# Optimization experiments

Hardware: AMD Instinct MI355X
Metric: run time of the kernel (lower is better)

## Reference

```python
import jax, jax.numpy as jnp
import numpy as np

NUM_GRAPHS = 1024

def setup_inputs() -> dict:
    key = jax.random.key(0)
    ks = jax.random.split(key, 6)
    N, E = 500000, 16000000
    x = jax.random.normal(ks[0], (N, 4), dtype=jnp.float32)
    edge_index = jax.random.randint(ks[1], (2, E), 0, N, dtype=jnp.int32)
    batch = jnp.sort(jax.random.randint(ks[2], (N,), 0, NUM_GRAPHS, dtype=jnp.int32))
    eps = jnp.zeros((), dtype=jnp.float32)
    W1 = jax.random.normal(ks[3], (4, 16), dtype=jnp.float32) * 0.5
    b1 = jnp.zeros((16,), dtype=jnp.float32)
    W2 = jax.random.normal(ks[4], (16, 4), dtype=jnp.float32) * 0.25
    b2 = jnp.zeros((4,), dtype=jnp.float32)
    return {"x": x, "edge_index": edge_index, "batch": batch,
            "eps": eps, "W1": W1, "b1": b1, "W2": W2, "b2": b2}

def reference(x, edge_index, batch, eps, W1, b1, W2, b2):
    N = x.shape[0]
    src, dst = edge_index[0], edge_index[1]
    # GINConv aggregation: sum of neighbor (source) features at each target node
    agg = jax.ops.segment_sum(x[src], dst, num_segments=N)  # [N, 4]
    h = (1.0 + eps) * x + agg
    # 2-layer MLP: Lin(4,16) -> ReLU -> Lin(16,4)
    h = jax.nn.relu(h @ W1 + b1) @ W2 + b2
    h = jax.nn.relu(h)
    # global_mean_pool over batch segment ids
    sums = jax.ops.segment_sum(h, batch, num_segments=NUM_GRAPHS)      # [G, 4]
    cnts = jax.ops.segment_sum(jnp.ones((N,), h.dtype), batch, num_segments=NUM_GRAPHS)
    pooled = sums / jnp.maximum(cnts, 1.0)[:, None]
    return jax.nn.log_softmax(pooled, axis=1)
```

## Files before the change

kernel.cpp:

```cpp
#include <hip/hip_runtime.h>

#define NUM_GRAPHS 1024
#define BIN_BITS 10
#define BIN_SIZE (1 << BIN_BITS)
#define EB 4096
#define STH 512
#define EPT 8
#define SWAVES 8
#define CURS 16
#define ACCTH 256
#define ACCW 4

typedef int v4i __attribute__((ext_vector_type(4)));

__device__ inline unsigned bf16_rn(float f) {
    unsigned u = __float_as_uint(f);
    return (u + 0x7FFFu + ((u >> 16) & 1u)) >> 16;
}
__global__ void prep_kernel(const float4* __restrict__ x, uint2* __restrict__ x16,
                            int N) {
    int i = blockIdx.x * blockDim.x + threadIdx.x;
    if (i < N) {
        float4 v = x[i];
        uint2 r;
        r.x = bf16_rn(v.x) | (bf16_rn(v.y) << 16);
        r.y = bf16_rn(v.z) | (bf16_rn(v.w) << 16);
        x16[i] = r;
    }
}

__global__ void __launch_bounds__(STH, 6) bin_scatter(const int* __restrict__ src,
                                                      const int* __restrict__ dst,
                                                      int* __restrict__ packed,
                                                      int* __restrict__ cursor,
                                                      int E, int cap, int nb) {
    __shared__ int hist[SWAVES][512];
    __shared__ int wbase[SWAVES][512];

    const int t = threadIdx.x;
    const int lane = t & 63;
    const int wave = t >> 6;
    const int b0 = blockIdx.x * EB;
    const int myBase = b0 + t * EPT;

    for (int j = t; j < SWAVES * 512; j += STH) (&hist[0][0])[j] = 0;
    __syncthreads();

    int dbuf[EPT], sbuf[EPT];
    const bool full = (myBase + EPT <= E);
    if (full) {
        *(int4*)(dbuf)     = *(const int4*)(dst + myBase);
        *(int4*)(dbuf + 4) = *(const int4*)(dst + myBase + 4);
        *(int4*)(sbuf)     = *(const int4*)(src + myBase);
        *(int4*)(sbuf + 4) = *(const int4*)(src + myBase + 4);
    } else {
#pragma unroll
        for (int i = 0; i < EPT; ++i) {
            int e = myBase + i;
            bool ok = e < E;
            dbuf[i] = ok ? dst[e] : 0;
            sbuf[i] = ok ? src[e] : 0;
        }
    }

    int pv[EPT];
    int bnlp[EPT];
#pragma unroll
    for (int k = 0; k < EPT; ++k) {
        int e = myBase + k;
        bool ok = full || (e < E);
        int d = dbuf[k];
        int bn = ((unsigned)d) >> BIN_BITS;
        pv[k] = ((d & (BIN_SIZE - 1)) << 19) | sbuf[k];
        unsigned long long m = __ballot(ok);
#pragma unroll
        for (int bb = 0; bb < 9; ++bb) {
            unsigned long long bm = __ballot((bn >> bb) & 1);
            m &= ((bn >> bb) & 1) ? bm : ~bm;
        }
        int rank = (int)__popcll(m & ((1ull << lane) - 1ull));
        int cnt  = (int)__popcll(m);
        int leader = __ffsll((unsigned long long)m) - 1;
        int old = hist[wave][bn];
        if (ok && lane == leader) hist[wave][bn] = old + cnt;
        bnlp[k] = ok ? ((bn << 16) | (old + rank)) : -1;
    }
    __syncthreads();

    {
        int c[SWAVES];
        int total = 0;
#pragma unroll
        for (int w = 0; w < SWAVES; ++w) { c[w] = hist[w][t]; total += c[w]; }
        int base = t * cap;
        if (t < nb && total > 0) base += atomicAdd(&cursor[t * CURS], total);
        int acc = base;
#pragma unroll
        for (int w = 0; w < SWAVES; ++w) { wbase[w][t] = acc; acc += c[w]; }
    }
    __syncthreads();

    if (full) {
#pragma unroll
        for (int k = 0; k < EPT; ++k) {
            int bn = ((unsigned)bnlp[k]) >> 16;
            int lp = bnlp[k] & 0xFFFF;
            int pos = wbase[wave][bn] + lp;
            if (pos < (bn + 1) * cap)
                packed[pos] = pv[k];
        }
    } else {
#pragma unroll
        for (int k = 0; k < EPT; ++k) {
            if (bnlp[k] >= 0) {
                int bn = ((unsigned)bnlp[k]) >> 16;
                int lp = bnlp[k] & 0xFFFF;
                int pos = wbase[wave][bn] + lp;
                if (pos < (bn + 1) * cap)
                    packed[pos] = pv[k];
            }
        }
    }
}

#define LOADR(B, PE, VM) do {                                              \
    int _i = (B) + lane * 4;                                               \
    if (_i + 3 < s1) {                                                     \
        v4i _p4 = __builtin_nontemporal_load((const v4i*)(packed + _i));   \
        PE[0] = _p4.x; PE[1] = _p4.y; PE[2] = _p4.z; PE[3] = _p4.w;        \
        VM = 0xF;                                                          \
    } else {                                                               \
        VM = 0;                                                            \
        PE[0] = (_i + 0 < s1) ? (VM |= 1, packed[_i + 0]) : 0;             \
        PE[1] = (_i + 1 < s1) ? (VM |= 2, packed[_i + 1]) : 0;             \
        PE[2] = (_i + 2 < s1) ? (VM |= 4, packed[_i + 2]) : 0;             \
        PE[3] = (_i + 3 < s1) ? (VM |= 8, packed[_i + 3]) : 0;             \
    }                                                                      \
} while (0)

#define GATHR(PE, G) do {                                                  \
    G[0] = x16[PE[0] & 0x7FFFF];                                           \
    G[1] = x16[PE[1] & 0x7FFFF];                                           \
    G[2] = x16[PE[2] & 0x7FFFF];                                           \
    G[3] = x16[PE[3] & 0x7FFFF];                                           \
} while (0)

#define PROCR(PE, G, VM) do {                                              \
    _Pragma("unroll")                                                      \
    for (int k = 0; k < 4; ++k) {                                          \
        int p = PE[k];                                                     \
        int dl = (((unsigned)p) >> 19) & (BIN_SIZE - 1);                   \
        unsigned long long m = ~0ull;                                      \
        _Pragma("unroll")                                                  \
        for (int bb = 0; bb < BIN_BITS; ++bb) {                            \
            unsigned long long bm = __ballot((dl >> bb) & 1);              \
            m &= ((dl >> bb) & 1) ? bm : ~bm;                              \
        }                                                                  \
        int rank = (int)__popcll(m & ((1ull << lane) - 1ull));             \
        float sc = ((VM >> k) & 1) ? 1.0f : 0.0f;                          \
        float v0 = __uint_as_float(G[k].x << 16) * sc;                     \
        float v1 = __uint_as_float(G[k].x & 0xFFFF0000u) * sc;             \
        float v2 = __uint_as_float(G[k].y << 16) * sc;                     \
        float v3 = __uint_as_float(G[k].y & 0xFFFF0000u) * sc;             \
        float4* pp = (float4*)&planes[wave][dl][0];                        \
        for (int pass = 0; __any(rank >= pass); ++pass) {                  \
            if (rank == pass) {                                            \
                float4 a = *pp;                                            \
                a.x += v0; a.y += v1; a.z += v2; a.w += v3;                \
                *pp = a;                                                   \
            }                                                              \
        }                                                                  \
    }                                                                      \
} while (0)

__global__ void __launch_bounds__(ACCTH) bin_accum_mlp_pool(
        const float4* __restrict__ x,
        const uint2* __restrict__ x16,
        const int* __restrict__ packed,
        const int* __restrict__ cursor,
        const int* __restrict__ batch,
        const float* __restrict__ eps_p,
        const float* __restrict__ W1, const float* __restrict__ b1,
        const float* __restrict__ W2, const float* __restrict__ b2,
        float* __restrict__ gsum, float* __restrict__ gcnt,
        int N, int cap) {
    __shared__ float planes[ACCW][BIN_SIZE][4];

    const int bin = blockIdx.x;
    const int t = threadIdx.x;
    const int lane = t & 63;
    const int wave = t >> 6;

    {
        float4* pz = (float4*)&planes[0][0][0];
        float4 z; z.x = 0.f; z.y = 0.f; z.z = 0.f; z.w = 0.f;
#pragma unroll
        for (int i = 0; i < 16; ++i) pz[t + i * ACCTH] = z;
    }
    __syncthreads();

    const int start = bin * cap;
    int cnt = cursor[bin * CURS];
    if (cnt > cap) cnt = cap;
    if (cnt < 0) cnt = 0;
    const int end = start + cnt;

    int seg = ((cnt + ACCW - 1) / ACCW + 3) & ~3;
    int s0 = start + wave * seg;
    int s1 = s0 + seg; if (s1 > end) s1 = end;

    if (s0 < s1) {
        int peA[4], peB[4], vmA, vmB;
        uint2 gA[4], gB[4];
        int b = s0;
        LOADR(b, peA, vmA);
        GATHR(peA, gA);
        for (;;) {
            int b1n = b + 256;
            if (b1n < s1) { LOADR(b1n, peB, vmB); GATHR(peB, gB); }
            PROCR(peA, gA, vmA);
            if (b1n >= s1) break;
            int b2n = b1n + 256;
            if (b2n < s1) { LOADR(b2n, peA, vmA); GATHR(peA, gA); }
            PROCR(peB, gB, vmB);
            if (b2n >= s1) break;
            b = b2n;
        }
    }
    __syncthreads();

    const float eps = eps_p[0];
    for (int half = 0; half < 4; ++half) {
        int node = t + half * ACCTH;
        float4 a = *(const float4*)&planes[0][node][0];
#pragma unroll
        for (int w = 1; w < ACCW; ++w) {
            float4 bq = *(const float4*)&planes[w][node][0];
            a.x += bq.x; a.y += bq.y; a.z += bq.z; a.w += bq.w;
        }

        int n = bin * BIN_SIZE + node;
        bool valid = n < N;
        float o0 = 0.f, o1 = 0.f, o2 = 0.f, o3 = 0.f;
        int g = -1;
        if (valid) {
            float4 xv = x[n];
            float h0 = (1.0f + eps) * xv.x + a.x;
            float h1 = (1.0f + eps) * xv.y + a.y;
            float h2 = (1.0f + eps) * xv.z + a.z;
            float h3 = (1.0f + eps) * xv.w + a.w;

            float tmp[16];
#pragma unroll
            for (int j = 0; j < 16; ++j) {
                float v = b1[j] + h0 * W1[j] + h1 * W1[16 + j] + h2 * W1[32 + j] + h3 * W1[48 + j];
                tmp[j] = v > 0.0f ? v : 0.0f;
            }
            float o[4];
#pragma unroll
            for (int j = 0; j < 4; ++j) {
                float v = b2[j];
#pragma unroll
                for (int k = 0; k < 16; ++k) v += tmp[k] * W2[k * 4 + j];
                o[j] = v > 0.0f ? v : 0.0f;
            }
            o0 = o[0]; o1 = o[1]; o2 = o[2]; o3 = o[3];
            g = batch[n];
        }

        int g0 = __shfl(g, 0);
        bool uni = __all(g == g0);
        if (uni && g0 >= 0) {
#pragma unroll
            for (int off = 32; off > 0; off >>= 1) {
                o0 += __shfl_down(o0, off);
                o1 += __shfl_down(o1, off);
                o2 += __shfl_down(o2, off);
                o3 += __shfl_down(o3, off);
            }
            if (lane == 0) {
                unsafeAtomicAdd(&gsum[(size_t)g0 * 4 + 0], o0);
                unsafeAtomicAdd(&gsum[(size_t)g0 * 4 + 1], o1);
                unsafeAtomicAdd(&gsum[(size_t)g0 * 4 + 2], o2);
                unsafeAtomicAdd(&gsum[(size_t)g0 * 4 + 3], o3);
                unsafeAtomicAdd(&gcnt[g0], 64.0f);
            }
        } else if (valid) {
            unsafeAtomicAdd(&gsum[(size_t)g * 4 + 0], o0);
            unsafeAtomicAdd(&gsum[(size_t)g * 4 + 1], o1);
            unsafeAtomicAdd(&gsum[(size_t)g * 4 + 2], o2);
            unsafeAtomicAdd(&gsum[(size_t)g * 4 + 3], o3);
            unsafeAtomicAdd(&gcnt[g], 1.0f);
        }
    }
}

__global__ void pool_softmax_kernel(const float* __restrict__ gsum,
                                    const float* __restrict__ gcnt,
                                    float* __restrict__ out) {
    int g = blockIdx.x * blockDim.x + threadIdx.x;
    if (g >= NUM_GRAPHS) return;
    float c = fmaxf(gcnt[g], 1.0f);
    float p0 = gsum[g * 4 + 0] / c;
    float p1 = gsum[g * 4 + 1] / c;
    float p2 = gsum[g * 4 + 2] / c;
    float p3 = gsum[g * 4 + 3] / c;
    float m = fmaxf(fmaxf(p0, p1), fmaxf(p2, p3));
    float s = expf(p0 - m) + expf(p1 - m) + expf(p2 - m) + expf(p3 - m);
    float lse = m + logf(s);
    out[g * 4 + 0] = p0 - lse;
    out[g * 4 + 1] = p1 - lse;
    out[g * 4 + 2] = p2 - lse;
    out[g * 4 + 3] = p3 - lse;
}

__global__ void edge_scatter_kernel(const float4* __restrict__ x,
                                    const int* __restrict__ src,
                                    const int* __restrict__ dst,
                                    float* __restrict__ agg,
                                    int E) {
    int t = blockIdx.x * blockDim.x + threadIdx.x;
    int e = t * 4;
    if (e + 3 < E) {
        int4 s = *(const int4*)(src + e);
        int4 d = *(const int4*)(dst + e);
        float4 xv;
        xv = x[s.x];
        unsafeAtomicAdd(&agg[(size_t)d.x * 4 + 0], xv.x);
        unsafeAtomicAdd(&agg[(size_t)d.x * 4 + 1], xv.y);
        unsafeAtomicAdd(&agg[(size_t)d.x * 4 + 2], xv.z);
        unsafeAtomicAdd(&agg[(size_t)d.x * 4 + 3], xv.w);
        xv = x[s.y];
        unsafeAtomicAdd(&agg[(size_t)d.y * 4 + 0], xv.x);
        unsafeAtomicAdd(&agg[(size_t)d.y * 4 + 1], xv.y);
        unsafeAtomicAdd(&agg[(size_t)d.y * 4 + 2], xv.z);
        unsafeAtomicAdd(&agg[(size_t)d.y * 4 + 3], xv.w);
        xv = x[s.z];
        unsafeAtomicAdd(&agg[(size_t)d.z * 4 + 0], xv.x);
        unsafeAtomicAdd(&agg[(size_t)d.z * 4 + 1], xv.y);
        unsafeAtomicAdd(&agg[(size_t)d.z * 4 + 2], xv.z);
        unsafeAtomicAdd(&agg[(size_t)d.z * 4 + 3], xv.w);
        xv = x[s.w];
        unsafeAtomicAdd(&agg[(size_t)d.w * 4 + 0], xv.x);
        unsafeAtomicAdd(&agg[(size_t)d.w * 4 + 1], xv.y);
        unsafeAtomicAdd(&agg[(size_t)d.w * 4 + 2], xv.z);
        unsafeAtomicAdd(&agg[(size_t)d.w * 4 + 3], xv.w);
    } else {
        for (int i = e; i < E; ++i) {
            int sv = src[i], dv = dst[i];
            float4 xv = x[sv];
            unsafeAtomicAdd(&agg[(size_t)dv * 4 + 0], xv.x);
            unsafeAtomicAdd(&agg[(size_t)dv * 4 + 1], xv.y);
            unsafeAtomicAdd(&agg[(size_t)dv * 4 + 2], xv.z);
            unsafeAtomicAdd(&agg[(size_t)dv * 4 + 3], xv.w);
        }
    }
}

__global__ void node_mlp_pool_kernel(const float4* __restrict__ x,
                                     const float4* __restrict__ agg,
                                     const int* __restrict__ batch,
                                     const float* __restrict__ eps_p,
                                     const float* __restrict__ W1,
                                     const float* __restrict__ b1,
                                     const float* __restrict__ W2,
                                     const float* __restrict__ b2,
                                     float* __restrict__ gsum,
                                     float* __restrict__ gcnt,
                                     int N) {
    int i = blockIdx.x * blockDim.x + threadIdx.x;
    bool valid = i < N;
    float o0 = 0.f, o1 = 0.f, o2 = 0.f, o3 = 0.f;
    int g = -1;
    if (valid) {
        float eps = eps_p[0];
        float4 xv = x[i];
        float4 av = agg[i];
        float h0 = (1.0f + eps) * xv.x + av.x;
        float h1 = (1.0f + eps) * xv.y + av.y;
        float h2 = (1.0f + eps) * xv.z + av.z;
        float h3 = (1.0f + eps) * xv.w + av.w;
        float tmp[16];
#pragma unroll
        for (int j = 0; j < 16; ++j) {
            float v = b1[j] + h0 * W1[j] + h1 * W1[16 + j] + h2 * W1[32 + j] + h3 * W1[48 + j];
            tmp[j] = v > 0.0f ? v : 0.0f;
        }
        float o[4];
#pragma unroll
        for (int j = 0; j < 4; ++j) {
            float v = b2[j];
#pragma unroll
            for (int k = 0; k < 16; ++k) v += tmp[k] * W2[k * 4 + j];
            o[j] = v > 0.0f ? v : 0.0f;
        }
        o0 = o[0]; o1 = o[1]; o2 = o[2]; o3 = o[3];
        g = batch[i];
    }
    int g0 = __shfl(g, 0);
    bool uni = __all(g == g0);
    if (uni && g0 >= 0) {
#pragma unroll
        for (int off = 32; off > 0; off >>= 1) {
            o0 += __shfl_down(o0, off);
            o1 += __shfl_down(o1, off);
            o2 += __shfl_down(o2, off);
            o3 += __shfl_down(o3, off);
        }
        if ((threadIdx.x & 63) == 0) {
            unsafeAtomicAdd(&gsum[(size_t)g0 * 4 + 0], o0);
            unsafeAtomicAdd(&gsum[(size_t)g0 * 4 + 1], o1);
            unsafeAtomicAdd(&gsum[(size_t)g0 * 4 + 2], o2);
            unsafeAtomicAdd(&gsum[(size_t)g0 * 4 + 3], o3);
            unsafeAtomicAdd(&gcnt[g0], 64.0f);
        }
    } else if (valid) {
        unsafeAtomicAdd(&gsum[(size_t)g * 4 + 0], o0);
        unsafeAtomicAdd(&gsum[(size_t)g * 4 + 1], o1);
        unsafeAtomicAdd(&gsum[(size_t)g * 4 + 2], o2);
        unsafeAtomicAdd(&gsum[(size_t)g * 4 + 3], o3);
        unsafeAtomicAdd(&gcnt[g], 1.0f);
    }
}

extern "C" void kernel_launch(void* const* d_in, const int* in_sizes, int n_in,
                              void* d_out, int out_size, void* d_ws, size_t ws_size,
                              hipStream_t stream) {
    const float* x     = (const float*)d_in[0];
    const int*   ei    = (const int*)d_in[1];
    const int*   batch = (const int*)d_in[2];
    const float* eps   = (const float*)d_in[3];
    const float* W1    = (const float*)d_in[4];
    const float* b1    = (const float*)d_in[5];
    const float* W2    = (const float*)d_in[6];
    const float* b2    = (const float*)d_in[7];

    const int N = in_sizes[0] / 4;
    const int E = in_sizes[1] / 2;
    const int* src = ei;
    const int* dst = ei + (size_t)E;

    const int nb = (N + BIN_SIZE - 1) >> BIN_BITS;
    const int epb = (E + nb - 1) / nb;
    int cap = epb + epb / 8 + 1024;
    cap = (cap + 3) & ~3;

    size_t x16_elems = ((size_t)2 * N + 3) & ~(size_t)3;
    size_t packed_elems = ((size_t)nb * cap + 3) & ~(size_t)3;
    size_t need = (x16_elems + packed_elems + 512 * CURS + NUM_GRAPHS * 5) * sizeof(float);

    if (nb <= 512 && N < (1 << 19) && need <= ws_size) {
        uint2* x16    = (uint2*)d_ws;
        int*   packed = (int*)d_ws + x16_elems;
        int*   cursor = packed + packed_elems;
        float* gsum   = (float*)(cursor + 512 * CURS);
        float* gcnt   = gsum + (size_t)NUM_GRAPHS * 4;

        (void)hipMemsetAsync(cursor, 0,
                             (512 * CURS + NUM_GRAPHS * 5) * sizeof(int), stream);

        prep_kernel<<<(N + 511) / 512, 512, 0, stream>>>((const float4*)x, x16, N);

        int nblocks_e = (E + EB - 1) / EB;
        bin_scatter<<<nblocks_e, STH, 0, stream>>>(src, dst, packed, cursor, E, cap, nb);

        bin_accum_mlp_pool<<<nb, ACCTH, 0, stream>>>(
            (const float4*)x, (const uint2*)x16, packed, cursor, batch, eps,
            W1, b1, W2, b2, gsum, gcnt, N, cap);

        pool_softmax_kernel<<<(NUM_GRAPHS + 255) / 256, 256, 0, stream>>>(
            gsum, gcnt, (float*)d_out);
    } else {
        float* agg  = (float*)d_ws;
        float* gsum = agg + (size_t)N * 4;
        float* gcnt = gsum + (size_t)NUM_GRAPHS * 4;
        size_t zero_bytes = ((size_t)N * 4 + NUM_GRAPHS * 5) * sizeof(float);
        (void)hipMemsetAsync(d_ws, 0, zero_bytes, stream);

        int e4 = (E + 3) / 4;
        edge_scatter_kernel<<<(e4 + 255) / 256, 256, 0, stream>>>(
            (const float4*)x, src, dst, agg, E);

        node_mlp_pool_kernel<<<(N + 255) / 256, 256, 0, stream>>>(
            (const float4*)x, (const float4*)agg, batch, eps, W1, b1, W2, b2,
            gsum, gcnt, N);

        pool_softmax_kernel<<<(NUM_GRAPHS + 255) / 256, 256, 0, stream>>>(
            gsum, gcnt, (float*)d_out);
    }
}
```

Baseline: 432.8 us.

## Fuse bf16 prep into bin_scatter and pre-reduce same-bin adds via shuffles

The separate prep kernel that converts x to packed bf16 is folded into the first threads of bin_scatter, removing one kernel launch. In the accumulation macro, lanes that share a destination row now combine their values with wave shuffles, so only the leader lane writes to shared memory. This replaces the previous serialized rank-by-rank LDS update loop. It adds shuffle-loop iterations proportional to the conflict count and a guard requiring enough scatter blocks to cover N.

```diff
diff --git a/kernel.cpp b/kernel.cpp
--- a/kernel.cpp
+++ b/kernel.cpp
@@ -17,23 +17,14 @@
     unsigned u = __float_as_uint(f);
     return (u + 0x7FFFu + ((u >> 16) & 1u)) >> 16;
 }
-__global__ void prep_kernel(const float4* __restrict__ x, uint2* __restrict__ x16,
-                            int N) {
-    int i = blockIdx.x * blockDim.x + threadIdx.x;
-    if (i < N) {
-        float4 v = x[i];
-        uint2 r;
-        r.x = bf16_rn(v.x) | (bf16_rn(v.y) << 16);
-        r.y = bf16_rn(v.z) | (bf16_rn(v.w) << 16);
-        x16[i] = r;
-    }
-}
-
-__global__ void __launch_bounds__(STH, 6) bin_scatter(const int* __restrict__ src,
+
+__global__ void __launch_bounds__(STH, 6) bin_scatter(const float4* __restrict__ x,
+                                                      uint2* __restrict__ x16,
+                                                      const int* __restrict__ src,
                                                       const int* __restrict__ dst,
                                                       int* __restrict__ packed,
                                                       int* __restrict__ cursor,
-                                                      int E, int cap, int nb) {
+                                                      int N, int E, int cap, int nb) {
     __shared__ int hist[SWAVES][512];
     __shared__ int wbase[SWAVES][512];
 
@@ -42,6 +33,17 @@
     const int wave = t >> 6;
     const int b0 = blockIdx.x * EB;
     const int myBase = b0 + t * EPT;
+
+    {
+        int nd = blockIdx.x * STH + t;
+        if (nd < N) {
+            float4 v = x[nd];
+            uint2 r;
+            r.x = bf16_rn(v.x) | (bf16_rn(v.y) << 16);
+            r.y = bf16_rn(v.z) | (bf16_rn(v.w) << 16);
+            x16[nd] = r;
+        }
+    }
 
     for (int j = t; j < SWAVES * 512; j += STH) (&hist[0][0])[j] = 0;
     __syncthreads();
@@ -162,13 +164,23 @@
         float v1 = __uint_as_float(G[k].x & 0xFFFF0000u) * sc;             \
         float v2 = __uint_as_float(G[k].y << 16) * sc;                     \
         float v3 = __uint_as_float(G[k].y & 0xFFFF0000u) * sc;             \
-        float4* pp = (float4*)&planes[wave][dl][0];                        \
-        for (int pass = 0; __any(rank >= pass); ++pass) {                  \
-            if (rank == pass) {                                            \
-                float4 a = *pp;                                            \
-                a.x += v0; a.y += v1; a.z += v2; a.w += v3;                \
-                *pp = a;                                                   \
-            }                                                              \
+                      \
+        unsigned long long rem =                                           \
+            (rank == 0) ? (m & ~(1ull << lane)) : 0ull;                    \
+        while (__any(rem != 0)) {                                          \
+            int srcl = rem ? (__ffsll((unsigned long long)rem) - 1) : 0;   \
+            float t0 = __shfl(v0, srcl);                                   \
+            float t1 = __shfl(v1, srcl);                                   \
+            float t2 = __shfl(v2, srcl);                                   \
+            float t3 = __shfl(v3, srcl);                                   \
+            if (rem) { v0 += t0; v1 += t1; v2 += t2; v3 += t3;             \
+                       rem &= rem - 1; }                                   \
+        }                                                                  \
+        if (rank == 0) {                                                   \
+            float4* pp = (float4*)&planes[wave][dl][0];                    \
+            float4 a = *pp;                                                \
+            a.x += v0; a.y += v1; a.z += v2; a.w += v3;                    \
+            *pp = a;                                                       \
         }                                                                  \
     }                                                                      \
 } while (0)
@@ -449,7 +461,10 @@
     size_t packed_elems = ((size_t)nb * cap + 3) & ~(size_t)3;
     size_t need = (x16_elems + packed_elems + 512 * CURS + NUM_GRAPHS * 5) * sizeof(float);
 
-    if (nb <= 512 && N < (1 << 19) && need <= ws_size) {
+    int nblocks_e = (E + EB - 1) / EB;
+    bool prep_ok = (size_t)nblocks_e * STH >= (size_t)N;
+
+    if (nb <= 512 && N < (1 << 19) && need <= ws_size && prep_ok) {
         uint2* x16    = (uint2*)d_ws;
         int*   packed = (int*)d_ws + x16_elems;
         int*   cursor = packed + packed_elems;
@@ -459,10 +474,8 @@
         (void)hipMemsetAsync(cursor, 0,
                              (512 * CURS + NUM_GRAPHS * 5) * sizeof(int), stream);
 
-        prep_kernel<<<(N + 511) / 512, 512, 0, stream>>>((const float4*)x, x16, N);
-
-        int nblocks_e = (E + EB - 1) / EB;
-        bin_scatter<<<nblocks_e, STH, 0, stream>>>(src, dst, packed, cursor, E, cap, nb);
+        bin_scatter<<<nblocks_e, STH, 0, stream>>>(
+            (const float4*)x, x16, src, dst, packed, cursor, N, E, cap, nb);
 
         bin_accum_mlp_pool<<<nb, ACCTH, 0, stream>>>(
             (const float4*)x, (const uint2*)x16, packed, cursor, batch, eps,
```

Result: no change. 429.6 us (-0.7%).

## Fuse GIN pipeline into one cooperative persistent kernel with grid syncs

Applied to the files above, without the earlier changes.

Replaces the memset, prep, binning scatter, accumulation and softmax launches with a single cooperative kernel. It uses grid-wide syncs between the phases and loops over chunks and bins persistently. This removes launch and memset overhead and inter-kernel gaps. In exchange, the persistent grid is capped at occupancy (at most 512 blocks), scatter runs with 4 waves per chunk instead of 8, and the double-buffered gather prefetch in accumulation is dropped. The non-cooperative fallback also folds the bf16 prep into bin_scatter.

```diff
diff --git a/kernel.cpp b/kernel.cpp
--- a/kernel.cpp
+++ b/kernel.cpp
@@ -1,126 +1,25 @@
 #include <hip/hip_runtime.h>
+#include <hip/hip_cooperative_groups.h>
+namespace cg = cooperative_groups;
 
 #define NUM_GRAPHS 1024
 #define BIN_BITS 10
 #define BIN_SIZE (1 << BIN_BITS)
+#define CURS 16
 #define EB 4096
 #define STH 512
 #define EPT 8
 #define SWAVES 8
-#define CURS 16
 #define ACCTH 256
 #define ACCW 4
+#define FEPT 8
+#define FCHK (ACCTH * FEPT)
 
 typedef int v4i __attribute__((ext_vector_type(4)));
 
 __device__ inline unsigned bf16_rn(float f) {
     unsigned u = __float_as_uint(f);
     return (u + 0x7FFFu + ((u >> 16) & 1u)) >> 16;
-}
-__global__ void prep_kernel(const float4* __restrict__ x, uint2* __restrict__ x16,
-                            int N) {
-    int i = blockIdx.x * blockDim.x + threadIdx.x;
-    if (i < N) {
-        float4 v = x[i];
-        uint2 r;
-        r.x = bf16_rn(v.x) | (bf16_rn(v.y) << 16);
-        r.y = bf16_rn(v.z) | (bf16_rn(v.w) << 16);
-        x16[i] = r;
-    }
-}
-
-__global__ void __launch_bounds__(STH, 6) bin_scatter(const int* __restrict__ src,
-                                                      const int* __restrict__ dst,
-                                                      int* __restrict__ packed,
-                                                      int* __restrict__ cursor,
-                                                      int E, int cap, int nb) {
-    __shared__ int hist[SWAVES][512];
-    __shared__ int wbase[SWAVES][512];
-
-    const int t = threadIdx.x;
-    const int lane = t & 63;
-    const int wave = t >> 6;
-    const int b0 = blockIdx.x * EB;
-    const int myBase = b0 + t * EPT;
-
-    for (int j = t; j < SWAVES * 512; j += STH) (&hist[0][0])[j] = 0;
-    __syncthreads();
-
-    int dbuf[EPT], sbuf[EPT];
-    const bool full = (myBase + EPT <= E);
-    if (full) {
-        *(int4*)(dbuf)     = *(const int4*)(dst + myBase);
-        *(int4*)(dbuf + 4) = *(const int4*)(dst + myBase + 4);
-        *(int4*)(sbuf)     = *(const int4*)(src + myBase);
-        *(int4*)(sbuf + 4) = *(const int4*)(src + myBase + 4);
-    } else {
-#pragma unroll
-        for (int i = 0; i < EPT; ++i) {
-            int e = myBase + i;
-            bool ok = e < E;
-            dbuf[i] = ok ? dst[e] : 0;
-            sbuf[i] = ok ? src[e] : 0;
-        }
-    }
-
-    int pv[EPT];
-    int bnlp[EPT];
-#pragma unroll
-    for (int k = 0; k < EPT; ++k) {
-        int e = myBase + k;
-        bool ok = full || (e < E);
-        int d = dbuf[k];
-        int bn = ((unsigned)d) >> BIN_BITS;
-        pv[k] = ((d & (BIN_SIZE - 1)) << 19) | sbuf[k];
-        unsigned long long m = __ballot(ok);
-#pragma unroll
-        for (int bb = 0; bb < 9; ++bb) {
-            unsigned long long bm = __ballot((bn >> bb) & 1);
-            m &= ((bn >> bb) & 1) ? bm : ~bm;
-        }
-        int rank = (int)__popcll(m & ((1ull << lane) - 1ull));
-        int cnt  = (int)__popcll(m);
-        int leader = __ffsll((unsigned long long)m) - 1;
-        int old = hist[wave][bn];
-        if (ok && lane == leader) hist[wave][bn] = old + cnt;
-        bnlp[k] = ok ? ((bn << 16) | (old + rank)) : -1;
-    }
-    __syncthreads();
-
-    {
-        int c[SWAVES];
-        int total = 0;
-#pragma unroll
-        for (int w = 0; w < SWAVES; ++w) { c[w] = hist[w][t]; total += c[w]; }
-        int base = t * cap;
-        if (t < nb && total > 0) base += atomicAdd(&cursor[t * CURS], total);
-        int acc = base;
-#pragma unroll
-        for (int w = 0; w < SWAVES; ++w) { wbase[w][t] = acc; acc += c[w]; }
-    }
-    __syncthreads();
-
-    if (full) {
-#pragma unroll
-        for (int k = 0; k < EPT; ++k) {
-            int bn = ((unsigned)bnlp[k]) >> 16;
-            int lp = bnlp[k] & 0xFFFF;
-            int pos = wbase[wave][bn] + lp;
-            if (pos < (bn + 1) * cap)
-                packed[pos] = pv[k];
-        }
-    } else {
-#pragma unroll
-        for (int k = 0; k < EPT; ++k) {
-            if (bnlp[k] >= 0) {
-                int bn = ((unsigned)bnlp[k]) >> 16;
-                int lp = bnlp[k] & 0xFFFF;
-                int pos = wbase[wave][bn] + lp;
-                if (pos < (bn + 1) * cap)
-                    packed[pos] = pv[k];
-            }
-        }
-    }
 }
 
 #define LOADR(B, PE, VM) do {                                              \
@@ -173,6 +72,345 @@
     }                                                                      \
 } while (0)
 
+__global__ void __launch_bounds__(ACCTH) fused_gin(
+        const float4* __restrict__ x, uint2* __restrict__ x16,
+        const int* __restrict__ src, const int* __restrict__ dst,
+        int* __restrict__ packed, int* __restrict__ cursor,
+        const int* __restrict__ batch, const float* __restrict__ eps_p,
+        const float* __restrict__ W1, const float* __restrict__ b1,
+        const float* __restrict__ W2, const float* __restrict__ b2,
+        float* __restrict__ gsum, float* __restrict__ gcnt,
+        float* __restrict__ out,
+        int N, int E, int cap, int nb) {
+    cg::grid_group grid = cg::this_grid();
+    __shared__ float planes[ACCW][BIN_SIZE][4];
+    int* hist  = (int*)&planes[0][0][0];
+    int* wbase = hist + ACCW * 512;
+
+    const int t = threadIdx.x;
+    const int lane = t & 63;
+    const int wave = t >> 6;
+    const int nblk = gridDim.x;
+    const int gid0 = blockIdx.x * ACCTH + t;
+    const int gstr = nblk * ACCTH;
+
+    for (int i = gid0; i < 512; i += gstr) cursor[i * CURS] = 0;
+    for (int i = gid0; i < NUM_GRAPHS * 4; i += gstr) gsum[i] = 0.0f;
+    for (int i = gid0; i < NUM_GRAPHS; i += gstr) gcnt[i] = 0.0f;
+    for (int i = gid0; i < N; i += gstr) {
+        float4 v = x[i];
+        uint2 r;
+        r.x = bf16_rn(v.x) | (bf16_rn(v.y) << 16);
+        r.y = bf16_rn(v.z) | (bf16_rn(v.w) << 16);
+        x16[i] = r;
+    }
+    grid.sync();
+
+    const int nchunks = (E + FCHK - 1) / FCHK;
+    for (int ch = blockIdx.x; ch < nchunks; ch += nblk) {
+        const int b0 = ch * FCHK;
+        const int myBase = b0 + t * FEPT;
+
+        for (int j = t; j < ACCW * 512; j += ACCTH) hist[j] = 0;
+        __syncthreads();
+
+        int dbuf[FEPT], sbuf[FEPT];
+        const bool full = (myBase + FEPT <= E);
+        if (full) {
+            *(int4*)(dbuf)     = *(const int4*)(dst + myBase);
+            *(int4*)(dbuf + 4) = *(const int4*)(dst + myBase + 4);
+            *(int4*)(sbuf)     = *(const int4*)(src + myBase);
+            *(int4*)(sbuf + 4) = *(const int4*)(src + myBase + 4);
+        } else {
+#pragma unroll
+            for (int i = 0; i < FEPT; ++i) {
+                int e = myBase + i;
+                bool ok = e < E;
+                dbuf[i] = ok ? dst[e] : 0;
+                sbuf[i] = ok ? src[e] : 0;
+            }
+        }
+
+        int pv[FEPT], bnlp[FEPT];
+#pragma unroll
+        for (int k = 0; k < FEPT; ++k) {
+            int e = myBase + k;
+            bool ok = full || (e < E);
+            int d = dbuf[k];
+            int bn = ((unsigned)d) >> BIN_BITS;
+            pv[k] = ((d & (BIN_SIZE - 1)) << 19) | sbuf[k];
+            unsigned long long m = __ballot(ok);
+#pragma unroll
+            for (int bb = 0; bb < 9; ++bb) {
+                unsigned long long bm = __ballot((bn >> bb) & 1);
+                m &= ((bn >> bb) & 1) ? bm : ~bm;
+            }
+            int rank = (int)__popcll(m & ((1ull << lane) - 1ull));
+            int cnt  = (int)__popcll(m);
+            int leader = __ffsll((unsigned long long)m) - 1;
+            int old = hist[wave * 512 + bn];
+            if (ok && lane == leader) hist[wave * 512 + bn] = old + cnt;
+            bnlp[k] = ok ? ((bn << 16) | (old + rank)) : -1;
+        }
+        __syncthreads();
+
+        for (int j = t; j < 512; j += ACCTH) {
+            int c0 = hist[0 * 512 + j], c1 = hist[1 * 512 + j];
+            int c2 = hist[2 * 512 + j], c3 = hist[3 * 512 + j];
+            int total = c0 + c1 + c2 + c3;
+            int base = j * cap;
+            if (j < nb && total > 0) base += atomicAdd(&cursor[j * CURS], total);
+            wbase[0 * 512 + j] = base;
+            wbase[1 * 512 + j] = base + c0;
+            wbase[2 * 512 + j] = base + c0 + c1;
+            wbase[3 * 512 + j] = base + c0 + c1 + c2;
+        }
+        __syncthreads();
+
+        if (full) {
+#pragma unroll
+            for (int k = 0; k < FEPT; ++k) {
+                int bn = ((unsigned)bnlp[k]) >> 16;
+                int lp = bnlp[k] & 0xFFFF;
+                int pos = wbase[wave * 512 + bn] + lp;
+                if (pos < (bn + 1) * cap)
+                    packed[pos] = pv[k];
+            }
+        } else {
+#pragma unroll
+            for (int k = 0; k < FEPT; ++k) {
+                if (bnlp[k] >= 0) {
+                    int bn = ((unsigned)bnlp[k]) >> 16;
+                    int lp = bnlp[k] & 0xFFFF;
+                    int pos = wbase[wave * 512 + bn] + lp;
+                    if (pos < (bn + 1) * cap)
+                        packed[pos] = pv[k];
+                }
+            }
+        }
+        __syncthreads();
+    }
+    __threadfence();
+    grid.sync();
+
+    for (int bin = blockIdx.x; bin < nb; bin += nblk) {
+        {
+            float4 z; z.x = 0.f; z.y = 0.f; z.z = 0.f; z.w = 0.f;
+            float4* pz = (float4*)&planes[0][0][0];
+#pragma unroll
+            for (int i = 0; i < 16; ++i) pz[t + i * ACCTH] = z;
+        }
+        __syncthreads();
+
+        const int startb = bin * cap;
+        int cnt = cursor[bin * CURS];
+        if (cnt > cap) cnt = cap;
+        if (cnt < 0) cnt = 0;
+        const int endb = startb + cnt;
+        int seg = ((cnt + ACCW - 1) / ACCW + 3) & ~3;
+        int s0 = startb + wave * seg;
+        int s1 = s0 + seg; if (s1 > endb) s1 = endb;
+
+        for (int b = s0; b < s1; b += 256) {
+            int pe[4]; int vm; uint2 g[4];
+            LOADR(b, pe, vm);
+            GATHR(pe, g);
+            PROCR(pe, g, vm);
+        }
+        __syncthreads();
+
+        const float eps = eps_p[0];
+        for (int hb = 0; hb < 4; ++hb) {
+            int node = t + hb * ACCTH;
+            float4 a = *(const float4*)&planes[0][node][0];
+#pragma unroll
+            for (int w = 1; w < ACCW; ++w) {
+                float4 bq = *(const float4*)&planes[w][node][0];
+                a.x += bq.x; a.y += bq.y; a.z += bq.z; a.w += bq.w;
+            }
+
+            int n = bin * BIN_SIZE + node;
+            bool valid = n < N;
+            float o0 = 0.f, o1 = 0.f, o2 = 0.f, o3 = 0.f;
+            int g = -1;
+            if (valid) {
+                float4 xv = x[n];
+                float h0 = (1.0f + eps) * xv.x + a.x;
+                float h1 = (1.0f + eps) * xv.y + a.y;
+                float h2 = (1.0f + eps) * xv.z + a.z;
+                float h3 = (1.0f + eps) * xv.w + a.w;
+
+                float tmp[16];
+#pragma unroll
+                for (int j = 0; j < 16; ++j) {
+                    float v = b1[j] + h0 * W1[j] + h1 * W1[16 + j] + h2 * W1[32 + j] + h3 * W1[48 + j];
+                    tmp[j] = v > 0.0f ? v : 0.0f;
+                }
+                float o[4];
+#pragma unroll
+                for (int j = 0; j < 4; ++j) {
+                    float v = b2[j];
+#pragma unroll
+                    for (int k = 0; k < 16; ++k) v += tmp[k] * W2[k * 4 + j];
+                    o[j] = v > 0.0f ? v : 0.0f;
+                }
+                o0 = o[0]; o1 = o[1]; o2 = o[2]; o3 = o[3];
+                g = batch[n];
+            }
+
+            int g0 = __shfl(g, 0);
+            bool uni = __all(g == g0);
+            if (uni && g0 >= 0) {
+#pragma unroll
+                for (int off = 32; off > 0; off >>= 1) {
+                    o0 += __shfl_down(o0, off);
+                    o1 += __shfl_down(o1, off);
+                    o2 += __shfl_down(o2, off);
+                    o3 += __shfl_down(o3, off);
+                }
+                if (lane == 0) {
+                    unsafeAtomicAdd(&gsum[(size_t)g0 * 4 + 0], o0);
+                    unsafeAtomicAdd(&gsum[(size_t)g0 * 4 + 1], o1);
+                    unsafeAtomicAdd(&gsum[(size_t)g0 * 4 + 2], o2);
+                    unsafeAtomicAdd(&gsum[(size_t)g0 * 4 + 3], o3);
+                    unsafeAtomicAdd(&gcnt[g0], 64.0f);
+                }
+            } else if (valid) {
+                unsafeAtomicAdd(&gsum[(size_t)g * 4 + 0], o0);
+                unsafeAtomicAdd(&gsum[(size_t)g * 4 + 1], o1);
+                unsafeAtomicAdd(&gsum[(size_t)g * 4 + 2], o2);
+                unsafeAtomicAdd(&gsum[(size_t)g * 4 + 3], o3);
+                unsafeAtomicAdd(&gcnt[g], 1.0f);
+            }
+        }
+        __syncthreads();
+    }
+    __threadfence();
+    grid.sync();
+
+    for (int g = gid0; g < NUM_GRAPHS; g += gstr) {
+        float c = fmaxf(unsafeAtomicAdd(&gcnt[g], 0.0f), 1.0f);
+        float p0 = unsafeAtomicAdd(&gsum[g * 4 + 0], 0.0f) / c;
+        float p1 = unsafeAtomicAdd(&gsum[g * 4 + 1], 0.0f) / c;
+        float p2 = unsafeAtomicAdd(&gsum[g * 4 + 2], 0.0f) / c;
+        float p3 = unsafeAtomicAdd(&gsum[g * 4 + 3], 0.0f) / c;
+        float m = fmaxf(fmaxf(p0, p1), fmaxf(p2, p3));
+        float s = expf(p0 - m) + expf(p1 - m) + expf(p2 - m) + expf(p3 - m);
+        float lse = m + logf(s);
+        out[g * 4 + 0] = p0 - lse;
+        out[g * 4 + 1] = p1 - lse;
+        out[g * 4 + 2] = p2 - lse;
+        out[g * 4 + 3] = p3 - lse;
+    }
+}
+
+__global__ void __launch_bounds__(STH, 6) bin_scatter(const float4* __restrict__ x,
+                                                      uint2* __restrict__ x16,
+                                                      const int* __restrict__ src,
+                                                      const int* __restrict__ dst,
+                                                      int* __restrict__ packed,
+                                                      int* __restrict__ cursor,
+                                                      int N, int E, int cap, int nb) {
+    __shared__ int hist[SWAVES][512];
+    __shared__ int wbase[SWAVES][512];
+
+    const int t = threadIdx.x;
+    const int lane = t & 63;
+    const int wave = t >> 6;
+    const int b0 = blockIdx.x * EB;
+    const int myBase = b0 + t * EPT;
+
+    {
+        int nd = blockIdx.x * STH + t;
+        if (nd < N) {
+            float4 v = x[nd];
+            uint2 r;
+            r.x = bf16_rn(v.x) | (bf16_rn(v.y) << 16);
+            r.y = bf16_rn(v.z) | (bf16_rn(v.w) << 16);
+            x16[nd] = r;
+        }
+    }
+
+    for (int j = t; j < SWAVES * 512; j += STH) (&hist[0][0])[j] = 0;
+    __syncthreads();
+
+    int dbuf[EPT], sbuf[EPT];
+    const bool full = (myBase + EPT <= E);
+    if (full) {
+        *(int4*)(dbuf)     = *(const int4*)(dst + myBase);
+        *(int4*)(dbuf + 4) = *(const int4*)(dst + myBase + 4);
+        *(int4*)(sbuf)     = *(const int4*)(src + myBase);
+        *(int4*)(sbuf + 4) = *(const int4*)(src + myBase + 4);
+    } else {
+#pragma unroll
+        for (int i = 0; i < EPT; ++i) {
+            int e = myBase + i;
+            bool ok = e < E;
+            dbuf[i] = ok ? dst[e] : 0;
+            sbuf[i] = ok ? src[e] : 0;
+        }
+    }
+
+    int pv[EPT];
+    int bnlp[EPT];
+#pragma unroll
+    for (int k = 0; k < EPT; ++k) {
+        int e = myBase + k;
+        bool ok = full || (e < E);
+        int d = dbuf[k];
+        int bn = ((unsigned)d) >> BIN_BITS;
+        pv[k] = ((d & (BIN_SIZE - 1)) << 19) | sbuf[k];
+        unsigned long long m = __ballot(ok);
+#pragma unroll
+        for (int bb = 0; bb < 9; ++bb) {
+            unsigned long long bm = __ballot((bn >> bb) & 1);
+            m &= ((bn >> bb) & 1) ? bm : ~bm;
+        }
+        int rank = (int)__popcll(m & ((1ull << lane) - 1ull));
+        int cnt  = (int)__popcll(m);
+        int leader = __ffsll((unsigned long long)m) - 1;
+        int old = hist[wave][bn];
+        if (ok && lane == leader) hist[wave][bn] = old + cnt;
+        bnlp[k] = ok ? ((bn << 16) | (old + rank)) : -1;
+    }
+    __syncthreads();
+
+    {
+        int c[SWAVES];
+        int total = 0;
+#pragma unroll
+        for (int w = 0; w < SWAVES; ++w) { c[w] = hist[w][t]; total += c[w]; }
+        int base = t * cap;
+        if (t < nb && total > 0) base += atomicAdd(&cursor[t * CURS], total);
+        int acc = base;
+#pragma unroll
+        for (int w = 0; w < SWAVES; ++w) { wbase[w][t] = acc; acc += c[w]; }
+    }
+    __syncthreads();
+
+    if (full) {
+#pragma unroll
+        for (int k = 0; k < EPT; ++k) {
+            int bn = ((unsigned)bnlp[k]) >> 16;
+            int lp = bnlp[k] & 0xFFFF;
+            int pos = wbase[wave][bn] + lp;
+            if (pos < (bn + 1) * cap)
+                packed[pos] = pv[k];
+        }
+    } else {
+#pragma unroll
+        for (int k = 0; k < EPT; ++k) {
+            if (bnlp[k] >= 0) {
+                int bn = ((unsigned)bnlp[k]) >> 16;
+                int lp = bnlp[k] & 0xFFFF;
+                int pos = wbase[wave][bn] + lp;
+                if (pos < (bn + 1) * cap)
+                    packed[pos] = pv[k];
+            }
+        }
+    }
+}
+
 __global__ void __launch_bounds__(ACCTH) bin_accum_mlp_pool(
         const float4* __restrict__ x,
         const uint2* __restrict__ x16,
@@ -192,46 +430,33 @@
     const int wave = t >> 6;
 
     {
+        float4 z; z.x = 0.f; z.y = 0.f; z.z = 0.f; z.w = 0.f;
         float4* pz = (float4*)&planes[0][0][0];
-        float4 z; z.x = 0.f; z.y = 0.f; z.z = 0.f; z.w = 0.f;
 #pragma unroll
         for (int i = 0; i < 16; ++i) pz[t + i * ACCTH] = z;
     }
     __syncthreads();
 
-    const int start = bin * cap;
+    const int startb = bin * cap;
     int cnt = cursor[bin * CURS];
     if (cnt > cap) cnt = cap;
     if (cnt < 0) cnt = 0;
-    const int end = start + cnt;
-
+    const int endb = startb + cnt;
     int seg = ((cnt + ACCW - 1) / ACCW + 3) & ~3;
-    int s0 = start + wave * seg;
-    int s1 = s0 + seg; if (s1 > end) s1 = end;
-
-    if (s0 < s1) {
-        int peA[4], peB[4], vmA, vmB;
-        uint2 gA[4], gB[4];
-        int b = s0;
-        LOADR(b, peA, vmA);
-        GATHR(peA, gA);
-        for (;;) {
-            int b1n = b + 256;
-            if (b1n < s1) { LOADR(b1n, peB, vmB); GATHR(peB, gB); }
-            PROCR(peA, gA, vmA);
-            if (b1n >= s1) break;
-            int b2n = b1n + 256;
-            if (b2n < s1) { LOADR(b2n, peA, vmA); GATHR(peA, gA); }
-            PROCR(peB, gB, vmB);
-            if (b2n >= s1) break;
-            b = b2n;
-        }
+    int s0 = startb + wave * seg;
+    int s1 = s0 + seg; if (s1 > endb) s1 = endb;
+
+    for (int b = s0; b < s1; b += 256) {
+        int pe[4]; int vm; uint2 g[4];
+        LOADR(b, pe, vm);
+        GATHR(pe, g);
+        PROCR(pe, g, vm);
     }
     __syncthreads();
 
     const float eps = eps_p[0];
-    for (int half = 0; half < 4; ++half) {
-        int node = t + half * ACCTH;
+    for (int hb = 0; hb < 4; ++hb) {
+        int node = t + hb * ACCTH;
         float4 a = *(const float4*)&planes[0][node][0];
 #pragma unroll
         for (int w = 1; w < ACCW; ++w) {
@@ -449,25 +674,52 @@
     size_t packed_elems = ((size_t)nb * cap + 3) & ~(size_t)3;
     size_t need = (x16_elems + packed_elems + 512 * CURS + NUM_GRAPHS * 5) * sizeof(float);
 
-    if (nb <= 512 && N < (1 << 19) && need <= ws_size) {
+    int nblocks_e = (E + EB - 1) / EB;
+    bool prep_ok = (size_t)nblocks_e * STH >= (size_t)N;
+
+    if (nb <= 512 && N < (1 << 19) && need <= ws_size && prep_ok) {
         uint2* x16    = (uint2*)d_ws;
         int*   packed = (int*)d_ws + x16_elems;
         int*   cursor = packed + packed_elems;
         float* gsum   = (float*)(cursor + 512 * CURS);
         float* gcnt   = gsum + (size_t)NUM_GRAPHS * 4;
 
+        static int coop_state = 0;
+        if (coop_state >= 0) {
+            int devId = 0;
+            (void)hipGetDevice(&devId);
+            hipDeviceProp_t prop;
+            (void)hipGetDeviceProperties(&prop, devId);
+            int maxb = 0;
+            (void)hipOccupancyMaxActiveBlocksPerMultiprocessor(&maxb, fused_gin, ACCTH, 0);
+            size_t cores = (size_t)maxb * (size_t)prop.multiProcessorCount;
+            if (prop.cooperativeLaunch && cores >= 1) {
+                int grid_n = (int)(cores < (size_t)512 ? cores : (size_t)512);
+                const float4* xf4 = (const float4*)x;
+                float* outp = (float*)d_out;
+                int Nv = N, Ev = E, capv = cap, nbv = nb;
+                void* args[] = { (void*)&xf4, (void*)&x16, (void*)&src, (void*)&dst,
+                                 (void*)&packed, (void*)&cursor, (void*)&batch,
+                                 (void*)&eps, (void*)&W1, (void*)&b1, (void*)&W2,
+                                 (void*)&b2, (void*)&gsum, (void*)&gcnt,
+                                 (void*)&outp, (void*)&Nv, (void*)&Ev,
+                                 (void*)&capv, (void*)&nbv };
+                hipError_t err = hipLaunchCooperativeKernel(
+                    fused_gin, dim3(grid_n), dim3(ACCTH), args, 0, stream);
+                if (err == hipSuccess) { coop_state = 1; return; }
+                coop_state = -1;
+            } else {
+                coop_state = -1;
+            }
+        }
+
         (void)hipMemsetAsync(cursor, 0,
                              (512 * CURS + NUM_GRAPHS * 5) * sizeof(int), stream);
-
-        prep_kernel<<<(N + 511) / 512, 512, 0, stream>>>((const float4*)x, x16, N);
-
-        int nblocks_e = (E + EB - 1) / EB;
-        bin_scatter<<<nblocks_e, STH, 0, stream>>>(src, dst, packed, cursor, E, cap, nb);
-
+        bin_scatter<<<nblocks_e, STH, 0, stream>>>(
+            (const float4*)x, x16, src, dst, packed, cursor, N, E, cap, nb);
         bin_accum_mlp_pool<<<nb, ACCTH, 0, stream>>>(
             (const float4*)x, (const uint2*)x16, packed, cursor, batch, eps,
             W1, b1, W2, b2, gsum, gcnt, N, cap);
-
         pool_softmax_kernel<<<(NUM_GRAPHS + 255) / 256, 256, 0, stream>>>(
             gsum, gcnt, (float*)d_out);
     } else {
@@ -480,11 +732,9 @@
         int e4 = (E + 3) / 4;
         edge_scatter_kernel<<<(e4 + 255) / 256, 256, 0, stream>>>(
             (const float4*)x, src, dst, agg, E);
-
         node_mlp_pool_kernel<<<(N + 255) / 256, 256, 0, stream>>>(
             (const float4*)x, (const float4*)agg, batch, eps, W1, b1, W2, b2,
             gsum, gcnt, N);
-
         pool_softmax_kernel<<<(NUM_GRAPHS + 255) / 256, 256, 0, stream>>>(
             gsum, gcnt, (float*)d_out);
     }
```

Result: slower. 772.4 us (+78.5%).

## Halve bin size to 512 nodes, fuse bf16 prep into scatter, simplify accumulate loop

Applied to the files above, without the earlier changes.

Destination bins shrink from 1024 to 512 nodes, so there are up to 1024 bins, twice as many accumulate blocks each with half the shared-memory planes, which should improve occupancy. The bf16 conversion of x is folded into the bin_scatter kernel to drop a launch, and the wbase array is removed by reusing hist for the per-bin bases. The double-buffered gather loop in the accumulator is replaced with a simple single-buffer loop, and the per-bin slack capacity is reduced. Risks include more scatter ballot rounds, more global atomics, the loss of software prefetch in the gather, and a higher chance of overflowing the tighter capacity.

```diff
diff --git a/kernel.cpp b/kernel.cpp
--- a/kernel.cpp
+++ b/kernel.cpp
@@ -1,8 +1,9 @@
 #include <hip/hip_runtime.h>
 
 #define NUM_GRAPHS 1024
-#define BIN_BITS 10
+#define BIN_BITS 9
 #define BIN_SIZE (1 << BIN_BITS)
+#define NBINS 1024
 #define EB 4096
 #define STH 512
 #define EPT 8
@@ -17,25 +18,15 @@
     unsigned u = __float_as_uint(f);
     return (u + 0x7FFFu + ((u >> 16) & 1u)) >> 16;
 }
-__global__ void prep_kernel(const float4* __restrict__ x, uint2* __restrict__ x16,
-                            int N) {
-    int i = blockIdx.x * blockDim.x + threadIdx.x;
-    if (i < N) {
-        float4 v = x[i];
-        uint2 r;
-        r.x = bf16_rn(v.x) | (bf16_rn(v.y) << 16);
-        r.y = bf16_rn(v.z) | (bf16_rn(v.w) << 16);
-        x16[i] = r;
-    }
-}
-
-__global__ void __launch_bounds__(STH, 6) bin_scatter(const int* __restrict__ src,
-                                                      const int* __restrict__ dst,
-                                                      int* __restrict__ packed,
-                                                      int* __restrict__ cursor,
-                                                      int E, int cap, int nb) {
-    __shared__ int hist[SWAVES][512];
-    __shared__ int wbase[SWAVES][512];
+
+__global__ void __launch_bounds__(STH) bin_scatter(const float4* __restrict__ x,
+                                                   uint2* __restrict__ x16,
+                                                   const int* __restrict__ src,
+                                                   const int* __restrict__ dst,
+                                                   int* __restrict__ packed,
+                                                   int* __restrict__ cursor,
+                                                   int N, int E, int cap, int nb) {
+    __shared__ int hist[SWAVES][NBINS];
 
     const int t = threadIdx.x;
     const int lane = t & 63;
@@ -43,7 +34,18 @@
     const int b0 = blockIdx.x * EB;
     const int myBase = b0 + t * EPT;
 
-    for (int j = t; j < SWAVES * 512; j += STH) (&hist[0][0])[j] = 0;
+    {
+        int nd = blockIdx.x * STH + t;
+        if (nd < N) {
+            float4 v = x[nd];
+            uint2 r;
+            r.x = bf16_rn(v.x) | (bf16_rn(v.y) << 16);
+            r.y = bf16_rn(v.z) | (bf16_rn(v.w) << 16);
+            x16[nd] = r;
+        }
+    }
+
+    for (int j = t; j < SWAVES * NBINS; j += STH) (&hist[0][0])[j] = 0;
     __syncthreads();
 
     int dbuf[EPT], sbuf[EPT];
@@ -74,7 +76,7 @@
         pv[k] = ((d & (BIN_SIZE - 1)) << 19) | sbuf[k];
         unsigned long long m = __ballot(ok);
 #pragma unroll
-        for (int bb = 0; bb < 9; ++bb) {
+        for (int bb = 0; bb < 10; ++bb) {
             unsigned long long bm = __ballot((bn >> bb) & 1);
             m &= ((bn >> bb) & 1) ? bm : ~bm;
         }
@@ -87,16 +89,16 @@
     }
     __syncthreads();
 
-    {
+    for (int j = t; j < NBINS; j += STH) {
         int c[SWAVES];
         int total = 0;
 #pragma unroll
-        for (int w = 0; w < SWAVES; ++w) { c[w] = hist[w][t]; total += c[w]; }
-        int base = t * cap;
-        if (t < nb && total > 0) base += atomicAdd(&cursor[t * CURS], total);
+        for (int w = 0; w < SWAVES; ++w) { c[w] = hist[w][j]; total += c[w]; }
+        int base = j * cap;
+        if (j < nb && total > 0) base += atomicAdd(&cursor[j * CURS], total);
         int acc = base;
 #pragma unroll
-        for (int w = 0; w < SWAVES; ++w) { wbase[w][t] = acc; acc += c[w]; }
+        for (int w = 0; w < SWAVES; ++w) { hist[w][j] = acc; acc += c[w]; }
     }
     __syncthreads();
 
@@ -105,7 +107,7 @@
         for (int k = 0; k < EPT; ++k) {
             int bn = ((unsigned)bnlp[k]) >> 16;
             int lp = bnlp[k] & 0xFFFF;
-            int pos = wbase[wave][bn] + lp;
+            int pos = hist[wave][bn] + lp;
             if (pos < (bn + 1) * cap)
                 packed[pos] = pv[k];
         }
@@ -115,7 +117,7 @@
             if (bnlp[k] >= 0) {
                 int bn = ((unsigned)bnlp[k]) >> 16;
                 int lp = bnlp[k] & 0xFFFF;
-                int pos = wbase[wave][bn] + lp;
+                int pos = hist[wave][bn] + lp;
                 if (pos < (bn + 1) * cap)
                     packed[pos] = pv[k];
             }
@@ -192,46 +194,33 @@
     const int wave = t >> 6;
 
     {
+        float4 z; z.x = 0.f; z.y = 0.f; z.z = 0.f; z.w = 0.f;
         float4* pz = (float4*)&planes[0][0][0];
-        float4 z; z.x = 0.f; z.y = 0.f; z.z = 0.f; z.w = 0.f;
-#pragma unroll
-        for (int i = 0; i < 16; ++i) pz[t + i * ACCTH] = z;
+#pragma unroll
+        for (int i = 0; i < 8; ++i) pz[t + i * ACCTH] = z;
     }
     __syncthreads();
 
-    const int start = bin * cap;
+    const int startb = bin * cap;
     int cnt = cursor[bin * CURS];
     if (cnt > cap) cnt = cap;
     if (cnt < 0) cnt = 0;
-    const int end = start + cnt;
-
+    const int endb = startb + cnt;
     int seg = ((cnt + ACCW - 1) / ACCW + 3) & ~3;
-    int s0 = start + wave * seg;
-    int s1 = s0 + seg; if (s1 > end) s1 = end;
-
-    if (s0 < s1) {
-        int peA[4], peB[4], vmA, vmB;
-        uint2 gA[4], gB[4];
-        int b = s0;
-        LOADR(b, peA, vmA);
-        GATHR(peA, gA);
-        for (;;) {
-            int b1n = b + 256;
-            if (b1n < s1) { LOADR(b1n, peB, vmB); GATHR(peB, gB); }
-            PROCR(peA, gA, vmA);
-            if (b1n >= s1) break;
-            int b2n = b1n + 256;
-            if (b2n < s1) { LOADR(b2n, peA, vmA); GATHR(peA, gA); }
-            PROCR(peB, gB, vmB);
-            if (b2n >= s1) break;
-            b = b2n;
-        }
+    int s0 = startb + wave * seg;
+    int s1 = s0 + seg; if (s1 > endb) s1 = endb;
+
+    for (int b = s0; b < s1; b += 256) {
+        int pe[4]; int vm; uint2 g[4];
+        LOADR(b, pe, vm);
+        GATHR(pe, g);
+        PROCR(pe, g, vm);
     }
     __syncthreads();
 
     const float eps = eps_p[0];
-    for (int half = 0; half < 4; ++half) {
-        int node = t + half * ACCTH;
+    for (int hb = 0; hb < 2; ++hb) {
+        int node = t + hb * ACCTH;
         float4 a = *(const float4*)&planes[0][node][0];
 #pragma unroll
         for (int w = 1; w < ACCW; ++w) {
@@ -442,27 +431,28 @@
 
     const int nb = (N + BIN_SIZE - 1) >> BIN_BITS;
     const int epb = (E + nb - 1) / nb;
-    int cap = epb + epb / 8 + 1024;
+    int cap = epb + epb / 16 + 512;
     cap = (cap + 3) & ~3;
 
     size_t x16_elems = ((size_t)2 * N + 3) & ~(size_t)3;
     size_t packed_elems = ((size_t)nb * cap + 3) & ~(size_t)3;
-    size_t need = (x16_elems + packed_elems + 512 * CURS + NUM_GRAPHS * 5) * sizeof(float);
-
-    if (nb <= 512 && N < (1 << 19) && need <= ws_size) {
+    size_t need = (x16_elems + packed_elems + NBINS * CURS + NUM_GRAPHS * 5) * sizeof(float);
+
+    int nblocks_e = (E + EB - 1) / EB;
+    bool prep_ok = (size_t)nblocks_e * STH >= (size_t)N;
+
+    if (nb <= NBINS && N < (1 << 19) && need <= ws_size && prep_ok) {
         uint2* x16    = (uint2*)d_ws;
         int*   packed = (int*)d_ws + x16_elems;
         int*   cursor = packed + packed_elems;
-        float* gsum   = (float*)(cursor + 512 * CURS);
+        float* gsum   = (float*)(cursor + NBINS * CURS);
         float* gcnt   = gsum + (size_t)NUM_GRAPHS * 4;
 
         (void)hipMemsetAsync(cursor, 0,
-                             (512 * CURS + NUM_GRAPHS * 5) * sizeof(int), stream);
-
-        prep_kernel<<<(N + 511) / 512, 512, 0, stream>>>((const float4*)x, x16, N);
-
-        int nblocks_e = (E + EB - 1) / EB;
-        bin_scatter<<<nblocks_e, STH, 0, stream>>>(src, dst, packed, cursor, E, cap, nb);
+                             (NBINS * CURS + NUM_GRAPHS * 5) * sizeof(int), stream);
+
+        bin_scatter<<<nblocks_e, STH, 0, stream>>>(
+            (const float4*)x, x16, src, dst, packed, cursor, N, E, cap, nb);
 
         bin_accum_mlp_pool<<<nb, ACCTH, 0, stream>>>(
             (const float4*)x, (const uint2*)x16, packed, cursor, batch, eps,
```

After: 541.6 us. 25.1% more time.
